# Kernel tuning notes

Measured on AMD Instinct MI355X. Metric: run time of the kernel, lower is better.

Reference implementation:

```python
import jax, jax.numpy as jnp
import numpy as np

T_STEPS = 128
N_RAYS = 16384
RAY_EXT = 10.0  # ray_ext_factor


def _posenc(x, n_freq=4):
    # x: (...,3) in [-1,1] -> (...,3 + 3*2*n_freq) = (...,27)
    feats = [x]
    for k in range(n_freq):
        f = (2.0 ** k) * jnp.pi
        feats.append(jnp.sin(f * x))
        feats.append(jnp.cos(f * x))
    return jnp.concatenate(feats, -1)


def _sh_deg2(d):
    # real spherical harmonics, degree 0 and 1 (4 coeffs), d unit vectors (...,3)
    x, y, z = d[..., 0], d[..., 1], d[..., 2]
    c0 = 0.28209479177387814
    c1 = 0.4886025119029199
    return jnp.stack([jnp.full_like(x, c0), c1 * y, c1 * z, c1 * x], -1)


def _forward(rays_o, rays_d, tnoise, aabb, W1, b1, W2, b2, Wc1, bc1, Wc2, bc2):
    # --- ray-AABB intersection (slab method), RayBundle.intersect_aabb ---
    inv_d = 1.0 / rays_d
    t0 = (aabb[0] - rays_o) * inv_d
    t1 = (aabb[1] - rays_o) * inv_d
    tnear = jnp.maximum(jnp.max(jnp.minimum(t0, t1), -1, keepdims=True), 0.0)  # (N,1)
    tfar = jnp.min(jnp.maximum(t0, t1), -1, keepdims=True)                      # (N,1)
    active = (tfar > tnear).astype(rays_o.dtype)  # active_mask; masking replaces compaction

    # --- StratifiedRayStepSampler: ts (T,N,1) ---
    T = tnoise.shape[0]
    base = (jnp.arange(T, dtype=rays_o.dtype)[:, None, None] + tnoise) / T
    ts = tnear[None] + (tfar - tnear)[None] * base
    xyz = rays_o[None] + ts * rays_d[None]  # (T,N,3)

    # --- vol.sample(xyz, ynm, return_color=True): density + color MLP ---
    xn = 2.0 * (xyz - aabb[0]) / (aabb[1] - aabb[0]) - 1.0
    enc = _posenc(xn)                             # (T,N,27)
    h = jax.nn.relu(enc @ W1 + b1)                # (T,N,64)
    dh = h @ W2 + b2                              # (T,N,16)
    sigma = jnp.exp(dh[..., :1])                  # (T,N,1) density
    feat = dh[..., 1:]                            # (T,N,15)
    dnorm = jnp.linalg.norm(rays_d, axis=-1, keepdims=True)  # (N,1)
    ynm = _sh_deg2(rays_d / dnorm)                # encode_raydir -> (N,4)
    ynm = jnp.broadcast_to(ynm[None], (T,) + ynm.shape)      # expand to (T,N,4)
    hc = jax.nn.relu(jnp.concatenate([feat, ynm], -1) @ Wc1 + bc1)
    rgb = jax.nn.sigmoid(hc @ Wc2 + bc2)          # (T,N,3)

    # --- integrate_timesteps: transmittance-weighted compositing ---
    tfinal = tfar * RAY_EXT
    delta = jnp.concatenate([ts[1:] - ts[:-1], tfinal[None] - ts[-1:]], 0)  # (T,N,1)
    sd = sigma * delta * dnorm[None]
    alpha = 1.0 - jnp.exp(-sd)
    trans = jnp.exp(-(jnp.cumsum(sd, 0) - sd))    # exclusive cumsum transmittance
    w = trans * alpha * active[None]              # (T,N,1); inactive rays -> zero maps

    color = jnp.sum(w * rgb, 0)                   # color_map  (N,3)
    alpha_map = jnp.sum(w, 0)                     # alpha_map  (N,1)
    return jnp.concatenate([color, alpha_map], -1)  # rgba (N,4)


def setup_inputs() -> dict:
    key = jax.random.key(0)
    ks = jax.random.split(key, 8)
    # origins on a sphere of radius 2.5 around the unit aabb, aimed at points inside it
    o = jax.random.normal(ks[0], (N_RAYS, 3), jnp.float32)
    o = 2.5 * o / jnp.linalg.norm(o, axis=-1, keepdims=True)
    tgt = jax.random.uniform(ks[1], (N_RAYS, 3), jnp.float32, -0.5, 0.5)
    d = tgt - o
    d = d / jnp.linalg.norm(d, axis=-1, keepdims=True)
    aabb = jnp.array([[-1.0, -1.0, -1.0], [1.0, 1.0, 1.0]], jnp.float32)
    tnoise = jax.random.uniform(ks[2], (T_STEPS, N_RAYS, 1), jnp.float32)
    s1, s2, s3, s4 = 27 ** -0.5, 64 ** -0.5, 19 ** -0.5, 64 ** -0.5
    return {
        'rays_o': o, 'rays_d': d, 'tnoise': tnoise, 'aabb': aabb,
        'W1': jax.random.normal(ks[3], (27, 64), jnp.float32) * s1,
        'b1': jnp.zeros((64,), jnp.float32),
        'W2': jax.random.normal(ks[4], (64, 16), jnp.float32) * (0.1 * s2),
        'b2': jnp.zeros((16,), jnp.float32),
        'Wc1': jax.random.normal(ks[5], (19, 64), jnp.float32) * s3,
        'bc1': jnp.zeros((64,), jnp.float32),
        'Wc2': jax.random.normal(ks[6], (64, 3), jnp.float32) * s4,
        'bc2': jnp.zeros((3,), jnp.float32),
    }


def reference(rays_o, rays_d, tnoise, aabb, W1, b1, W2, b2, Wc1, bc1, Wc2, bc2):
    return _forward(rays_o, rays_d, tnoise, aabb, W1, b1, W2, b2, Wc1, bc1, Wc2, bc2)
```

## Files before the change

### kernel.cpp

```cpp
#include <hip/hip_runtime.h>
#include <stdint.h>

#define N_RAYS  16384
#define T_STEPS 128
#define RPW   16
#define WAVES 8
#define TSEG  16

typedef _Float16 half8  __attribute__((ext_vector_type(8)));
typedef __fp16   fp16x2 __attribute__((ext_vector_type(2)));
typedef float    float4_ __attribute__((ext_vector_type(4)));
typedef uint32_t uint2_  __attribute__((ext_vector_type(2)));

#define H8_W1   0
#define H8_W2   256
#define H8_WC1  384
#define H8_WC2  640
#define BC2_F32_OFF 3072

__device__ __forceinline__ uint32_t pkr(float a, float b) {
    fp16x2 h = __builtin_amdgcn_cvt_pkrtz(fmaxf(a, 0.f), fmaxf(b, 0.f));
    return __builtin_bit_cast(uint32_t, h);
}
__device__ __forceinline__ uint32_t pk(float a, float b) {
    fp16x2 h = __builtin_amdgcn_cvt_pkrtz(a, b);
    return __builtin_bit_cast(uint32_t, h);
}

__global__ void prep_weights(const float* __restrict__ W1, const float* __restrict__ b1,
                             const float* __restrict__ W2, const float* __restrict__ b2,
                             const float* __restrict__ Wc1, const float* __restrict__ bc1,
                             const float* __restrict__ Wc2, const float* __restrict__ bc2,
                             void* __restrict__ ws) {
    _Float16* wh = (_Float16*)ws;
    float*    wf = (float*)ws;
    int fl = blockIdx.x * 64 + threadIdx.x;
    if (fl < 12 * 64) {
        int frag = fl >> 6, lane = fl & 63;
        int mm = lane & 15, q = lane >> 4;
        if (frag < 4) {
            int tau = frag;
            int n = tau * 16 + mm;
            for (int j = 0; j < 8; ++j) {
                float w;
                if (j < 6)      w = W1[(3 + 6 * q + j) * 64 + n];
                else if (j == 6) w = (q == 0) ? W1[0 * 64 + n] : (q == 1) ? W1[2 * 64 + n] : 0.f;
                else             w = (q == 0) ? W1[1 * 64 + n] : (q == 1) ? b1[n] : 0.f;
                wh[(H8_W1 + tau * 64 + lane) * 8 + j] = (_Float16)w;
            }
        } else if (frag < 6) {
            int kap = frag - 4;
            for (int j = 0; j < 8; ++j) {
                int k = kap * 32 + q * 8 + j;
                wh[(H8_W2 + kap * 64 + lane) * 8 + j] = (_Float16)W2[k * 16 + mm];
            }
        } else if (frag < 10) {
            int tau = frag - 6;
            int nh = tau * 16 + mm;
            for (int j = 0; j < 8; ++j) {
                int s = q * 8 + j;
                float w;
                if (s == 0)       w = Wc1[15 * 64 + nh];
                else if (s <= 15) w = Wc1[(s - 1) * 64 + nh];
                else if (s <= 18) w = Wc1[s * 64 + nh];
                else if (s == 19) w = bc1[nh];
                else              w = 0.f;
                wh[(H8_WC1 + tau * 64 + lane) * 8 + j] = (_Float16)w;
            }
        } else {
            int kap = frag - 10;
            for (int j = 0; j < 8; ++j) {
                int k = kap * 32 + q * 8 + j;
                wh[(H8_WC2 + kap * 64 + lane) * 8 + j] =
                    (_Float16)((mm < 3) ? Wc2[k * 3 + mm] : 0.f);
            }
        }
    }
    if (blockIdx.x == 0 && threadIdx.x < 16)
        wf[BC2_F32_OFF + threadIdx.x] = (threadIdx.x < 3) ? bc2[threadIdx.x] : 0.f;
}

__global__ __launch_bounds__(512, 4)
void render_kernel(const float* __restrict__ rays_o, const float* __restrict__ rays_d,
                   const float* __restrict__ tnoise, const float* __restrict__ aabb,
                   const void* __restrict__ ws, float* __restrict__ out) {
    __shared__ __align__(16) _Float16 sH[WAVES][8 * 16 * 8];
    __shared__ __align__(16) _Float16 sF[WAVES][4 * 16 * 8];
    __shared__ float sComb[WAVES][RPW][5];

    const int tid  = threadIdx.x;
    const int wv   = tid >> 6;
    const int lane = tid & 63;
    const int m    = lane & 15;
    const int q    = lane >> 4;
    const int r    = blockIdx.x * RPW + m;

    const half8* wsv = (const half8*)ws;
    half8 fW1[4], fW2[2], fWc1[4], fWc2[2];
    #pragma unroll
    for (int i = 0; i < 4; ++i) fW1[i]  = wsv[H8_W1  + i * 64 + lane];
    #pragma unroll
    for (int i = 0; i < 2; ++i) fW2[i]  = wsv[H8_W2  + i * 64 + lane];
    #pragma unroll
    for (int i = 0; i < 4; ++i) fWc1[i] = wsv[H8_WC1 + i * 64 + lane];
    #pragma unroll
    for (int i = 0; i < 2; ++i) fWc2[i] = wsv[H8_WC2 + i * 64 + lane];
    const float4_ binit = ((const float4_*)((const float*)ws + BC2_F32_OFF))[q];

    float o0 = rays_o[r * 3 + 0], o1 = rays_o[r * 3 + 1], o2 = rays_o[r * 3 + 2];
    float d0 = rays_d[r * 3 + 0], d1 = rays_d[r * 3 + 1], d2 = rays_d[r * 3 + 2];
    float a00 = aabb[0], a01 = aabb[1], a02 = aabb[2];
    float a10 = aabb[3], a11 = aabb[4], a12 = aabb[5];

    float i0 = 1.0f / d0, i1 = 1.0f / d1, i2 = 1.0f / d2;
    float u0 = (a00 - o0) * i0, v0 = (a10 - o0) * i0;
    float u1 = (a01 - o1) * i1, v1 = (a11 - o1) * i1;
    float u2 = (a02 - o2) * i2, v2 = (a12 - o2) * i2;
    float tnear = fmaxf(fmaxf(fmaxf(fminf(u0, v0), fminf(u1, v1)), fminf(u2, v2)), 0.0f);
    float tfar  = fminf(fminf(fmaxf(u0, v0), fmaxf(u1, v1)), fmaxf(u2, v2));
    bool active = (tfar > tnear);
    float dt = tfar - tnear;

    float dn  = sqrtf(d0 * d0 + d1 * d1 + d2 * d2);
    float idn = 1.0f / dn;
    const float c0sh = 0.28209479177387814f;
    const float c1sh = 0.4886025119029199f;

    float sc0 = 2.0f / (a10 - a00), of0 = -a00 * sc0 - 1.0f;
    float sc1 = 2.0f / (a11 - a01), of1 = -a01 * sc1 - 1.0f;
    float sc2 = 2.0f / (a12 - a02), of2 = -a02 * sc2 - 1.0f;

    _Float16* Hb = sH[wv];
    _Float16* Fb = sF[wv];
    _Float16*       hw  = &Hb[((q >> 1) * 16 + m) * 8 + 4 * (q & 1)];
    const _Float16* hr  = &Hb[(q * 16 + m) * 8];
    _Float16*       fw  = &Fb[((q >> 1) * 16 + m) * 8 + 4 * (q & 1)];
    const _Float16* fr  = &Fb[(q * 16 + m) * 8];

    if (q == 2) {
        half8 c = {};
        c[0] = (_Float16)(c1sh * d1 * idn);
        c[1] = (_Float16)(c1sh * d2 * idn);
        c[2] = (_Float16)(c1sh * d0 * idn);
        c[3] = (_Float16)1.0f;
        *(half8*)fr = c;
    } else if (q == 3) {
        half8 z = {};
        *(half8*)fr = z;
    }

    const float fk = 3.14159265358979323846f * (float)(1 << q);
    const float4_ z4 = {0.f, 0.f, 0.f, 0.f};

    float trans = 1.0f, sdtot = 0.0f, wacc = 0.0f;
    float cacc0 = 0.0f, cacc1 = 0.0f, cacc2 = 0.0f;

    const int tbase = wv * TSEG;
    float n_cur = tnoise[tbase * N_RAYS + r];

    #pragma unroll 1
    for (int t = tbase; t < tbase + TSEG; ++t) {
        float n_nxt = (t < T_STEPS - 1) ? tnoise[(t + 1) * N_RAYS + r] : 0.0f;
        float ts  = fmaf(dt, ((float)t + n_cur) * (1.0f / 128.0f), tnear);
        float tsn = fmaf(dt, ((float)(t + 1) + n_nxt) * (1.0f / 128.0f), tnear);
        float delta = (t < T_STEPS - 1) ? (tsn - ts) : fmaf(tfar, 10.0f, -ts);
        n_cur = n_nxt;

        float xn0 = fmaf(fmaf(ts, d0, o0), sc0, of0);
        float xn1 = fmaf(fmaf(ts, d1, o1), sc1, of1);
        float xn2 = fmaf(fmaf(ts, d2, o2), sc2, of2);

        float s0 = __sinf(fk * xn0), s1 = __sinf(fk * xn1), s2 = __sinf(fk * xn2);
        float cA = __cosf(fk * xn0), cB = __cosf(fk * xn1), cC = __cosf(fk * xn2);
        float e6 = (q == 0) ? xn0 : (q == 1) ? xn2 : 0.0f;
        float e7 = (q == 0) ? xn1 : (q == 1) ? 1.0f : 0.0f;
        union { uint32_t u[4]; half8 h; } xf_;
        xf_.u[0] = pk(s0, s1); xf_.u[1] = pk(s2, cA);
        xf_.u[2] = pk(cB, cC); xf_.u[3] = pk(e6, e7);
        half8 xf = xf_.h;

        float4_ h0 = __builtin_amdgcn_mfma_f32_16x16x32_f16(fW1[0], xf, z4, 0, 0, 0);
        float4_ h1 = __builtin_amdgcn_mfma_f32_16x16x32_f16(fW1[1], xf, z4, 0, 0, 0);
        float4_ h2 = __builtin_amdgcn_mfma_f32_16x16x32_f16(fW1[2], xf, z4, 0, 0, 0);
        float4_ h3 = __builtin_amdgcn_mfma_f32_16x16x32_f16(fW1[3], xf, z4, 0, 0, 0);

        {
            uint2_ w;
            w.x = pkr(h0.x, h0.y); w.y = pkr(h0.z, h0.w); *(uint2_*)(hw + 0 * 256) = w;
            w.x = pkr(h1.x, h1.y); w.y = pkr(h1.z, h1.w); *(uint2_*)(hw + 1 * 256) = w;
            w.x = pkr(h2.x, h2.y); w.y = pkr(h2.z, h2.w); *(uint2_*)(hw + 2 * 256) = w;
            w.x = pkr(h3.x, h3.y); w.y = pkr(h3.z, h3.w); *(uint2_*)(hw + 3 * 256) = w;
        }

        half8 hb0 = *(const half8*)(hr + 0);
        half8 hb1 = *(const half8*)(hr + 512);
        float4_ dh = __builtin_amdgcn_mfma_f32_16x16x32_f16(fW2[0], hb0, z4, 0, 0, 0);
        dh = __builtin_amdgcn_mfma_f32_16x16x32_f16(fW2[1], hb1, dh, 0, 0, 0);

        {
            float f0 = (q == 0) ? c0sh : dh.x;
            uint2_ w;
            w.x = pk(f0, dh.y); w.y = pk(dh.z, dh.w);
            *(uint2_*)fw = w;
        }

        half8 fb = *(const half8*)fr;
        float4_ g0 = __builtin_amdgcn_mfma_f32_16x16x32_f16(fWc1[0], fb, z4, 0, 0, 0);
        float4_ g1 = __builtin_amdgcn_mfma_f32_16x16x32_f16(fWc1[1], fb, z4, 0, 0, 0);
        float4_ g2 = __builtin_amdgcn_mfma_f32_16x16x32_f16(fWc1[2], fb, z4, 0, 0, 0);
        float4_ g3 = __builtin_amdgcn_mfma_f32_16x16x32_f16(fWc1[3], fb, z4, 0, 0, 0);

        {
            uint2_ w;
            w.x = pkr(g0.x, g0.y); w.y = pkr(g0.z, g0.w); *(uint2_*)(hw + 0 * 256) = w;
            w.x = pkr(g1.x, g1.y); w.y = pkr(g1.z, g1.w); *(uint2_*)(hw + 1 * 256) = w;
            w.x = pkr(g2.x, g2.y); w.y = pkr(g2.z, g2.w); *(uint2_*)(hw + 2 * 256) = w;
            w.x = pkr(g3.x, g3.y); w.y = pkr(g3.z, g3.w); *(uint2_*)(hw + 3 * 256) = w;
        }

        half8 cb0 = *(const half8*)(hr + 0);
        half8 cb1 = *(const half8*)(hr + 512);
        float4_ rgbp = __builtin_amdgcn_mfma_f32_16x16x32_f16(fWc2[0], cb0, binit, 0, 0, 0);
        rgbp = __builtin_amdgcn_mfma_f32_16x16x32_f16(fWc2[1], cb1, rgbp, 0, 0, 0);

        float sigma = __expf(dh.x);
        float sd = sigma * delta * dn;
        float e = __expf(-sd);
        float alpha = 1.0f - e;
        float w = trans * alpha;
        float rr = 1.0f / (1.0f + __expf(-rgbp.x));
        float rg = 1.0f / (1.0f + __expf(-rgbp.y));
        float rb = 1.0f / (1.0f + __expf(-rgbp.z));
        cacc0 = fmaf(w, rr, cacc0);
        cacc1 = fmaf(w, rg, cacc1);
        cacc2 = fmaf(w, rb, cacc2);
        wacc += w;
        trans *= e;
        sdtot += sd;
    }

    if (q == 0) {
        sComb[wv][m][0] = sdtot;
        sComb[wv][m][1] = wacc;
        sComb[wv][m][2] = cacc0;
        sComb[wv][m][3] = cacc1;
        sComb[wv][m][4] = cacc2;
    }
    __syncthreads();

    if (tid < RPW) {
        float P = 1.0f, C0 = 0.0f, C1 = 0.0f, C2 = 0.0f, WS = 0.0f;
        #pragma unroll
        for (int s = 0; s < WAVES; ++s) {
            C0 = fmaf(P, sComb[s][tid][2], C0);
            C1 = fmaf(P, sComb[s][tid][3], C1);
            C2 = fmaf(P, sComb[s][tid][4], C2);
            WS = fmaf(P, sComb[s][tid][1], WS);
            P *= __expf(-sComb[s][tid][0]);
        }
        float act = active ? 1.0f : 0.0f;
        const int rg = blockIdx.x * RPW + tid;
        out[rg * 4 + 0] = C0 * act;
        out[rg * 4 + 1] = C1 * act;
        out[rg * 4 + 2] = C2 * act;
        out[rg * 4 + 3] = WS * act;
    }
}

extern "C" void kernel_launch(void* const* d_in, const int* in_sizes, int n_in,
                              void* d_out, int out_size, void* d_ws, size_t ws_size,
                              hipStream_t stream) {
    const float* rays_o = (const float*)d_in[0];
    const float* rays_d = (const float*)d_in[1];
    const float* tnoise = (const float*)d_in[2];
    const float* aabb   = (const float*)d_in[3];
    const float* W1  = (const float*)d_in[4];
    const float* b1  = (const float*)d_in[5];
    const float* W2  = (const float*)d_in[6];
    const float* b2  = (const float*)d_in[7];
    const float* Wc1 = (const float*)d_in[8];
    const float* bc1 = (const float*)d_in[9];
    const float* Wc2 = (const float*)d_in[10];
    const float* bc2 = (const float*)d_in[11];

    prep_weights<<<dim3(12), dim3(64), 0, stream>>>(W1, b1, W2, b2, Wc1, bc1, Wc2, bc2, d_ws);

    dim3 grid(N_RAYS / RPW);
    dim3 block(WAVES * 64);
    render_kernel<<<grid, block, 0, stream>>>(rays_o, rays_d, tnoise, aabb, d_ws,
                                              (float*)d_out);
}
```

Measured before the change: 140.1 us.

## Interleave two timesteps per iteration with double-buffered LDS and cheaper transcendentals

The time loop now processes two timesteps per iteration. Each MLP stage runs for both steps before the next stage starts, using separate double-buffered LDS scratch so independent MFMA chains can overlap their latencies. Sin and cos use the hardware instructions directly, with the frequency and the 1/(2π) revolution scaling folded into per-lane constants. ReLU is applied as a packed fp16 max, the sigmoid uses the hardware reciprocal, and compositing runs only on the lanes that own it. The occupancy hint drops from 4 to 3 blocks to allow more registers, at the cost of fewer resident waves.

Result: faster. 124.2 us (-11.3%).

```diff
diff --git a/kernel.cpp b/kernel.cpp
--- a/kernel.cpp
+++ b/kernel.cpp
@@ -18,13 +18,15 @@
 #define H8_WC2  640
 #define BC2_F32_OFF 3072
 
-__device__ __forceinline__ uint32_t pkr(float a, float b) {
-    fp16x2 h = __builtin_amdgcn_cvt_pkrtz(fmaxf(a, 0.f), fmaxf(b, 0.f));
-    return __builtin_bit_cast(uint32_t, h);
-}
 __device__ __forceinline__ uint32_t pk(float a, float b) {
     fp16x2 h = __builtin_amdgcn_cvt_pkrtz(a, b);
     return __builtin_bit_cast(uint32_t, h);
+}
+__device__ __forceinline__ uint32_t pkr(float a, float b) {
+    fp16x2 h = __builtin_amdgcn_cvt_pkrtz(a, b);
+    fp16x2 z = {(__fp16)0.f, (__fp16)0.f};
+    fp16x2 m = __builtin_elementwise_max(h, z);
+    return __builtin_bit_cast(uint32_t, m);
 }
 
 __global__ void prep_weights(const float* __restrict__ W1, const float* __restrict__ b1,
@@ -80,12 +82,12 @@
         wf[BC2_F32_OFF + threadIdx.x] = (threadIdx.x < 3) ? bc2[threadIdx.x] : 0.f;
 }
 
-__global__ __launch_bounds__(512, 4)
+__global__ __launch_bounds__(512, 3)
 void render_kernel(const float* __restrict__ rays_o, const float* __restrict__ rays_d,
                    const float* __restrict__ tnoise, const float* __restrict__ aabb,
                    const void* __restrict__ ws, float* __restrict__ out) {
-    __shared__ __align__(16) _Float16 sH[WAVES][8 * 16 * 8];
-    __shared__ __align__(16) _Float16 sF[WAVES][4 * 16 * 8];
+    __shared__ __align__(16) _Float16 sH[WAVES][2][1024];
+    __shared__ __align__(16) _Float16 sF[WAVES][2][512];
     __shared__ float sComb[WAVES][RPW][5];
 
     const int tid  = threadIdx.x;
@@ -120,22 +122,32 @@
     float tfar  = fminf(fminf(fmaxf(u0, v0), fmaxf(u1, v1)), fmaxf(u2, v2));
     bool active = (tfar > tnear);
     float dt = tfar - tnear;
+    float dt128 = dt * (1.0f / 128.0f);
 
     float dn  = sqrtf(d0 * d0 + d1 * d1 + d2 * d2);
     float idn = 1.0f / dn;
     const float c0sh = 0.28209479177387814f;
     const float c1sh = 0.4886025119029199f;
 
+    float qs = 0.5f * (float)(1 << q);
     float sc0 = 2.0f / (a10 - a00), of0 = -a00 * sc0 - 1.0f;
     float sc1 = 2.0f / (a11 - a01), of1 = -a01 * sc1 - 1.0f;
     float sc2 = 2.0f / (a12 - a02), of2 = -a02 * sc2 - 1.0f;
-
-    _Float16* Hb = sH[wv];
-    _Float16* Fb = sF[wv];
-    _Float16*       hw  = &Hb[((q >> 1) * 16 + m) * 8 + 4 * (q & 1)];
-    const _Float16* hr  = &Hb[(q * 16 + m) * 8];
-    _Float16*       fw  = &Fb[((q >> 1) * 16 + m) * 8 + 4 * (q & 1)];
-    const _Float16* fr  = &Fb[(q * 16 + m) * 8];
+    float scq0 = sc0 * qs, ofq0 = of0 * qs;
+    float scq1 = sc1 * qs, ofq1 = of1 * qs;
+    float scq2 = sc2 * qs, ofq2 = of2 * qs;
+
+    _Float16*       hwp[2];
+    const _Float16* hrp[2];
+    _Float16*       fwp[2];
+    const _Float16* frp[2];
+    #pragma unroll
+    for (int p = 0; p < 2; ++p) {
+        hwp[p] = &sH[wv][p][((q >> 1) * 16 + m) * 8 + 4 * (q & 1)];
+        hrp[p] = &sH[wv][p][(q * 16 + m) * 8];
+        fwp[p] = &sF[wv][p][((q >> 1) * 16 + m) * 8 + 4 * (q & 1)];
+        frp[p] = &sF[wv][p][(q * 16 + m) * 8];
+    }
 
     if (q == 2) {
         half8 c = {};
@@ -143,100 +155,126 @@
         c[1] = (_Float16)(c1sh * d2 * idn);
         c[2] = (_Float16)(c1sh * d0 * idn);
         c[3] = (_Float16)1.0f;
-        *(half8*)fr = c;
+        *(half8*)frp[0] = c;
+        *(half8*)frp[1] = c;
     } else if (q == 3) {
         half8 z = {};
-        *(half8*)fr = z;
-    }
-
-    const float fk = 3.14159265358979323846f * (float)(1 << q);
+        *(half8*)frp[0] = z;
+        *(half8*)frp[1] = z;
+    }
+
     const float4_ z4 = {0.f, 0.f, 0.f, 0.f};
+    const bool q0 = (q == 0), q1 = (q == 1);
 
     float trans = 1.0f, sdtot = 0.0f, wacc = 0.0f;
     float cacc0 = 0.0f, cacc1 = 0.0f, cacc2 = 0.0f;
 
     const int tbase = wv * TSEG;
-    float n_cur = tnoise[tbase * N_RAYS + r];
+    float nA = tnoise[(tbase + 0) * N_RAYS + r];
+    float nB = tnoise[(tbase + 1) * N_RAYS + r];
 
     #pragma unroll 1
-    for (int t = tbase; t < tbase + TSEG; ++t) {
-        float n_nxt = (t < T_STEPS - 1) ? tnoise[(t + 1) * N_RAYS + r] : 0.0f;
-        float ts  = fmaf(dt, ((float)t + n_cur) * (1.0f / 128.0f), tnear);
-        float tsn = fmaf(dt, ((float)(t + 1) + n_nxt) * (1.0f / 128.0f), tnear);
-        float delta = (t < T_STEPS - 1) ? (tsn - ts) : fmaf(tfar, 10.0f, -ts);
-        n_cur = n_nxt;
-
-        float xn0 = fmaf(fmaf(ts, d0, o0), sc0, of0);
-        float xn1 = fmaf(fmaf(ts, d1, o1), sc1, of1);
-        float xn2 = fmaf(fmaf(ts, d2, o2), sc2, of2);
-
-        float s0 = __sinf(fk * xn0), s1 = __sinf(fk * xn1), s2 = __sinf(fk * xn2);
-        float cA = __cosf(fk * xn0), cB = __cosf(fk * xn1), cC = __cosf(fk * xn2);
-        float e6 = (q == 0) ? xn0 : (q == 1) ? xn2 : 0.0f;
-        float e7 = (q == 0) ? xn1 : (q == 1) ? 1.0f : 0.0f;
-        union { uint32_t u[4]; half8 h; } xf_;
-        xf_.u[0] = pk(s0, s1); xf_.u[1] = pk(s2, cA);
-        xf_.u[2] = pk(cB, cC); xf_.u[3] = pk(e6, e7);
-        half8 xf = xf_.h;
-
-        float4_ h0 = __builtin_amdgcn_mfma_f32_16x16x32_f16(fW1[0], xf, z4, 0, 0, 0);
-        float4_ h1 = __builtin_amdgcn_mfma_f32_16x16x32_f16(fW1[1], xf, z4, 0, 0, 0);
-        float4_ h2 = __builtin_amdgcn_mfma_f32_16x16x32_f16(fW1[2], xf, z4, 0, 0, 0);
-        float4_ h3 = __builtin_amdgcn_mfma_f32_16x16x32_f16(fW1[3], xf, z4, 0, 0, 0);
-
-        {
+    for (int tt = 0; tt < TSEG; tt += 2) {
+        const int t0 = tbase + tt, t1 = t0 + 1;
+        float nC = (t0 + 2 < T_STEPS) ? tnoise[(t0 + 2) * N_RAYS + r] : 0.0f;
+        float nD = (t0 + 3 < T_STEPS) ? tnoise[(t0 + 3) * N_RAYS + r] : 0.0f;
+        float ts0 = fmaf((float)t0 + nA, dt128, tnear);
+        float ts1 = fmaf((float)t1 + nB, dt128, tnear);
+        float ts2 = fmaf((float)(t0 + 2) + nC, dt128, tnear);
+        float tsP[2]    = {ts0, ts1};
+        float deltaP[2];
+        deltaP[0] = ts1 - ts0;
+        deltaP[1] = (t1 < T_STEPS - 1) ? (ts2 - ts1) : fmaf(tfar, 10.0f, -ts1);
+        nA = nC; nB = nD;
+
+        float4_ dhP[2], rgbP[2];
+
+        #pragma unroll
+        for (int p = 0; p < 2; ++p) {
+            float x = fmaf(tsP[p], d0, o0);
+            float y = fmaf(tsP[p], d1, o1);
+            float z = fmaf(tsP[p], d2, o2);
+            float xr0 = fmaf(x, scq0, ofq0);
+            float xr1 = fmaf(y, scq1, ofq1);
+            float xr2 = fmaf(z, scq2, ofq2);
+            float s0 = __builtin_amdgcn_sinf(xr0);
+            float s1 = __builtin_amdgcn_sinf(xr1);
+            float s2 = __builtin_amdgcn_sinf(xr2);
+            float cA = __builtin_amdgcn_cosf(xr0);
+            float cB = __builtin_amdgcn_cosf(xr1);
+            float cC = __builtin_amdgcn_cosf(xr2);
+            float e6 = q0 ? (xr0 + xr0) : (q1 ? xr2 : 0.0f);
+            float e7 = q0 ? (xr1 + xr1) : (q1 ? 1.0f : 0.0f);
+            union { uint32_t u[4]; half8 h; } xf_;
+            xf_.u[0] = pk(s0, s1); xf_.u[1] = pk(s2, cA);
+            xf_.u[2] = pk(cB, cC); xf_.u[3] = pk(e6, e7);
+            half8 xf = xf_.h;
+
+            float4_ h0 = __builtin_amdgcn_mfma_f32_16x16x32_f16(fW1[0], xf, z4, 0, 0, 0);
+            float4_ h1 = __builtin_amdgcn_mfma_f32_16x16x32_f16(fW1[1], xf, z4, 0, 0, 0);
+            float4_ h2 = __builtin_amdgcn_mfma_f32_16x16x32_f16(fW1[2], xf, z4, 0, 0, 0);
+            float4_ h3 = __builtin_amdgcn_mfma_f32_16x16x32_f16(fW1[3], xf, z4, 0, 0, 0);
             uint2_ w;
-            w.x = pkr(h0.x, h0.y); w.y = pkr(h0.z, h0.w); *(uint2_*)(hw + 0 * 256) = w;
-            w.x = pkr(h1.x, h1.y); w.y = pkr(h1.z, h1.w); *(uint2_*)(hw + 1 * 256) = w;
-            w.x = pkr(h2.x, h2.y); w.y = pkr(h2.z, h2.w); *(uint2_*)(hw + 2 * 256) = w;
-            w.x = pkr(h3.x, h3.y); w.y = pkr(h3.z, h3.w); *(uint2_*)(hw + 3 * 256) = w;
-        }
-
-        half8 hb0 = *(const half8*)(hr + 0);
-        half8 hb1 = *(const half8*)(hr + 512);
-        float4_ dh = __builtin_amdgcn_mfma_f32_16x16x32_f16(fW2[0], hb0, z4, 0, 0, 0);
-        dh = __builtin_amdgcn_mfma_f32_16x16x32_f16(fW2[1], hb1, dh, 0, 0, 0);
-
-        {
-            float f0 = (q == 0) ? c0sh : dh.x;
+            w.x = pkr(h0.x, h0.y); w.y = pkr(h0.z, h0.w); *(uint2_*)(hwp[p] + 0 * 256) = w;
+            w.x = pkr(h1.x, h1.y); w.y = pkr(h1.z, h1.w); *(uint2_*)(hwp[p] + 1 * 256) = w;
+            w.x = pkr(h2.x, h2.y); w.y = pkr(h2.z, h2.w); *(uint2_*)(hwp[p] + 2 * 256) = w;
+            w.x = pkr(h3.x, h3.y); w.y = pkr(h3.z, h3.w); *(uint2_*)(hwp[p] + 3 * 256) = w;
+        }
+
+        #pragma unroll
+        for (int p = 0; p < 2; ++p) {
+            half8 hb0 = *(const half8*)(hrp[p] + 0);
+            half8 hb1 = *(const half8*)(hrp[p] + 512);
+            float4_ dh = __builtin_amdgcn_mfma_f32_16x16x32_f16(fW2[0], hb0, z4, 0, 0, 0);
+            dh = __builtin_amdgcn_mfma_f32_16x16x32_f16(fW2[1], hb1, dh, 0, 0, 0);
+            dhP[p] = dh;
+            float f0 = q0 ? c0sh : dh.x;
             uint2_ w;
             w.x = pk(f0, dh.y); w.y = pk(dh.z, dh.w);
-            *(uint2_*)fw = w;
-        }
-
-        half8 fb = *(const half8*)fr;
-        float4_ g0 = __builtin_amdgcn_mfma_f32_16x16x32_f16(fWc1[0], fb, z4, 0, 0, 0);
-        float4_ g1 = __builtin_amdgcn_mfma_f32_16x16x32_f16(fWc1[1], fb, z4, 0, 0, 0);
-        float4_ g2 = __builtin_amdgcn_mfma_f32_16x16x32_f16(fWc1[2], fb, z4, 0, 0, 0);
-        float4_ g3 = __builtin_amdgcn_mfma_f32_16x16x32_f16(fWc1[3], fb, z4, 0, 0, 0);
-
-        {
+            *(uint2_*)fwp[p] = w;
+        }
+
+        #pragma unroll
+        for (int p = 0; p < 2; ++p) {
+            half8 fb = *(const half8*)frp[p];
+            float4_ g0 = __builtin_amdgcn_mfma_f32_16x16x32_f16(fWc1[0], fb, z4, 0, 0, 0);
+            float4_ g1 = __builtin_amdgcn_mfma_f32_16x16x32_f16(fWc1[1], fb, z4, 0, 0, 0);
+            float4_ g2 = __builtin_amdgcn_mfma_f32_16x16x32_f16(fWc1[2], fb, z4, 0, 0, 0);
+            float4_ g3 = __builtin_amdgcn_mfma_f32_16x16x32_f16(fWc1[3], fb, z4, 0, 0, 0);
             uint2_ w;
-            w.x = pkr(g0.x, g0.y); w.y = pkr(g0.z, g0.w); *(uint2_*)(hw + 0 * 256) = w;
-            w.x = pkr(g1.x, g1.y); w.y = pkr(g1.z, g1.w); *(uint2_*)(hw + 1 * 256) = w;
-            w.x = pkr(g2.x, g2.y); w.y = pkr(g2.z, g2.w); *(uint2_*)(hw + 2 * 256) = w;
-            w.x = pkr(g3.x, g3.y); w.y = pkr(g3.z, g3.w); *(uint2_*)(hw + 3 * 256) = w;
-        }
-
-        half8 cb0 = *(const half8*)(hr + 0);
-        half8 cb1 = *(const half8*)(hr + 512);
-        float4_ rgbp = __builtin_amdgcn_mfma_f32_16x16x32_f16(fWc2[0], cb0, binit, 0, 0, 0);
-        rgbp = __builtin_amdgcn_mfma_f32_16x16x32_f16(fWc2[1], cb1, rgbp, 0, 0, 0);
-
-        float sigma = __expf(dh.x);
-        float sd = sigma * delta * dn;
-        float e = __expf(-sd);
-        float alpha = 1.0f - e;
-        float w = trans * alpha;
-        float rr = 1.0f / (1.0f + __expf(-rgbp.x));
-        float rg = 1.0f / (1.0f + __expf(-rgbp.y));
-        float rb = 1.0f / (1.0f + __expf(-rgbp.z));
-        cacc0 = fmaf(w, rr, cacc0);
-        cacc1 = fmaf(w, rg, cacc1);
-        cacc2 = fmaf(w, rb, cacc2);
-        wacc += w;
-        trans *= e;
-        sdtot += sd;
+            w.x = pkr(g0.x, g0.y); w.y = pkr(g0.z, g0.w); *(uint2_*)(hwp[p] + 0 * 256) = w;
+            w.x = pkr(g1.x, g1.y); w.y = pkr(g1.z, g1.w); *(uint2_*)(hwp[p] + 1 * 256) = w;
+            w.x = pkr(g2.x, g2.y); w.y = pkr(g2.z, g2.w); *(uint2_*)(hwp[p] + 2 * 256) = w;
+            w.x = pkr(g3.x, g3.y); w.y = pkr(g3.z, g3.w); *(uint2_*)(hwp[p] + 3 * 256) = w;
+        }
+
+        #pragma unroll
+        for (int p = 0; p < 2; ++p) {
+            half8 cb0 = *(const half8*)(hrp[p] + 0);
+            half8 cb1 = *(const half8*)(hrp[p] + 512);
+            float4_ rgbp = __builtin_amdgcn_mfma_f32_16x16x32_f16(fWc2[0], cb0, binit, 0, 0, 0);
+            rgbP[p] = __builtin_amdgcn_mfma_f32_16x16x32_f16(fWc2[1], cb1, rgbp, 0, 0, 0);
+        }
+
+        if (q == 0) {
+            #pragma unroll
+            for (int p = 0; p < 2; ++p) {
+                float sigma = __expf(dhP[p].x);
+                float sd = sigma * deltaP[p] * dn;
+                float e = __expf(-sd);
+                float alpha = 1.0f - e;
+                float w = trans * alpha;
+                float rr = __builtin_amdgcn_rcpf(1.0f + __expf(-rgbP[p].x));
+                float rg = __builtin_amdgcn_rcpf(1.0f + __expf(-rgbP[p].y));
+                float rb = __builtin_amdgcn_rcpf(1.0f + __expf(-rgbP[p].z));
+                cacc0 = fmaf(w, rr, cacc0);
+                cacc1 = fmaf(w, rg, cacc1);
+                cacc2 = fmaf(w, rb, cacc2);
+                wacc += w;
+                trans *= e;
+                sdtot += sd;
+            }
+        }
     }
 
     if (q == 0) {
```
